# Kernel tuning notes

Measured on AMD Instinct MI355X. Metric: run time of the kernel, lower is better.

The kernel has to match this reference:

```python
import jax, jax.numpy as jnp
import numpy as np

NUM_NODES = 100000
NUM_EDGES = 1600000
NUM_GRAPHS = 64
NUM_FEATURES = 128
DIM = 128
OUTPUT_SIZE = 16


def setup_inputs() -> dict:
    key = jax.random.key(0)
    ks = jax.random.split(key, 7)
    features = jax.random.normal(ks[0], (NUM_NODES, NUM_FEATURES), dtype=jnp.float32)
    W1 = jax.random.normal(ks[1], (NUM_FEATURES, DIM), dtype=jnp.float32) / np.sqrt(NUM_FEATURES)
    W2 = jax.random.normal(ks[2], (DIM, DIM), dtype=jnp.float32) / np.sqrt(DIM)
    W3 = jax.random.normal(ks[3], (DIM, OUTPUT_SIZE), dtype=jnp.float32) / np.sqrt(DIM)
    src = jax.random.randint(ks[4], (NUM_EDGES,), 0, NUM_NODES, dtype=jnp.int32)
    dst = jax.random.randint(ks[5], (NUM_EDGES,), 0, NUM_NODES, dtype=jnp.int32)
    graph_ids = jnp.sort(jax.random.randint(ks[6], (NUM_NODES,), 0, NUM_GRAPHS, dtype=jnp.int32))
    return {"features": features, "W1": W1, "W2": W2, "W3": W3,
            "src": src, "dst": dst, "graph_ids": graph_ids}


def _graph_conv(x, W, src, dst, num_nodes):
    # DGL GraphConv, norm='none', bias=False: h_v = sum_{u -> v} (x_u @ W)
    xw = x @ W                      # [N, dim]
    msg = xw[src]                   # gather per edge [E, dim]
    return jax.ops.segment_sum(msg, dst, num_segments=num_nodes)


def reference(features, W1, W2, W3, src, dst, graph_ids):
    n = features.shape[0]
    h = jax.nn.relu(_graph_conv(features, W1, src, dst, n))  # conv1 + ReLU
    h = _graph_conv(h, W2, src, dst, n)                      # conv2
    # dgl.mean_nodes: per-graph mean over nodes
    sums = jax.ops.segment_sum(h, graph_ids, num_segments=NUM_GRAPHS)          # [G, dim]
    counts = jax.ops.segment_sum(jnp.ones((n,), h.dtype), graph_ids,
                                 num_segments=NUM_GRAPHS)                       # [G]
    pooled = sums / jnp.maximum(counts, 1.0)[:, None]
    out = pooled @ W3                                         # fc1 (no bias)
    return jax.nn.sigmoid(out)                                # torch.sigmoid activation
```

## Files before the change

### kernel.cpp

```cpp
#include <hip/hip_runtime.h>

#define NXCD 8
#define PA_NB 256
#define CSLOT 32
#define OVCAP 65536

typedef short bf16x8 __attribute__((ext_vector_type(8)));
typedef float f32x4  __attribute__((ext_vector_type(4)));
typedef unsigned int u32x2 __attribute__((ext_vector_type(2)));
typedef unsigned int u32x4 __attribute__((ext_vector_type(4)));

union U4S8 { uint4 u; u32x4 v; bf16x8 s; };

__device__ __forceinline__ unsigned int f2bf(float f) {
    unsigned int u = __float_as_uint(f);
    return (u + 0x7fffu + ((u >> 16) & 1u)) >> 16;
}
__device__ __forceinline__ float bflo(unsigned int u) { return __uint_as_float(u << 16); }
__device__ __forceinline__ float bfhi(unsigned int u) { return __uint_as_float(u & 0xffff0000u); }

__device__ __forceinline__ f32x4 nt_ld_f4(const float4* p) {
    return __builtin_nontemporal_load((const f32x4*)p);
}
__device__ __forceinline__ u32x2 nt_ld_u2(const uint2* p) {
    return __builtin_nontemporal_load((const u32x2*)p);
}
__device__ __forceinline__ unsigned int nt_ld_u(const unsigned int* p) {
    return __builtin_nontemporal_load(p);
}

__global__ __launch_bounds__(256) void fconv(
    const float4* __restrict__ F4, uint4* __restrict__ B4, long long n8)
{
    long long t = (long long)blockIdx.x * 256 + threadIdx.x;
    if (t >= n8) return;
    f32x4 a = nt_ld_f4(&F4[2 * t]);
    f32x4 b = nt_ld_f4(&F4[2 * t + 1]);
    uint4 o;
    o.x = f2bf(a.x) | (f2bf(a.y) << 16);
    o.y = f2bf(a.z) | (f2bf(a.w) << 16);
    o.z = f2bf(b.x) | (f2bf(b.y) << 16);
    o.w = f2bf(b.z) | (f2bf(b.w) << 16);
    B4[t] = o;
}

__global__ __launch_bounds__(256) void fillfix_xcd(
    const int* __restrict__ src, const int* __restrict__ dst,
    int* __restrict__ cnt, int* __restrict__ col,
    int* __restrict__ ovd, int* __restrict__ ovs, int* __restrict__ ov_cnt,
    int E, int N)
{
    int x  = blockIdx.x & (NXCD - 1);
    int bi = blockIdx.x >> 3;
    int K  = gridDim.x >> 3;
    int chunk = (N + NXCD - 1) / NXCD;
    int lo = x * chunk;
    int hi = lo + chunk; if (hi > N) hi = N;
    for (int e = bi * 256 + threadIdx.x; e < E; e += K * 256) {
        int d = dst[e];
        int s = src[e];
        if (d >= lo && d < hi) {
            int pos = atomicAdd(&cnt[d], 1);
            if (pos < CSLOT) {
                col[(size_t)d * CSLOT + pos] = s;
            } else {
                int op = atomicAdd(ov_cnt, 1);
                if (op < OVCAP) { ovd[op] = d; ovs[op] = s; }
            }
        }
    }
}

__global__ __launch_bounds__(256) void edge_pa(
    const int* __restrict__ src, const int* __restrict__ dst,
    const int* __restrict__ gid, unsigned int* __restrict__ PA32, int E, int N)
{
    int x  = blockIdx.x & (NXCD - 1);
    int bi = blockIdx.x >> 3;
    int K  = gridDim.x >> 3;
    int chunk = (N + NXCD - 1) / NXCD;
    int lo = x * chunk;
    int hi = lo + chunk; if (hi > N) hi = N;
    for (int e = bi * 256 + threadIdx.x; e < E; e += K * 256) {
        int s = src[e];
        int d = dst[e];
        if (s >= lo && s < hi) {
            int g = gid[d];
            atomicAdd(&PA32[(size_t)s * 16 + (g >> 2)], 1u << ((g & 3) * 8));
        }
    }
}

__global__ __launch_bounds__(256) void csr_agg_bf16(
    const uint4* __restrict__ X, const int* __restrict__ cnt,
    const int* __restrict__ col,
    const int* __restrict__ ovd, const int* __restrict__ ovs,
    const int* __restrict__ ov_cnt,
    uint4* __restrict__ T, int N)
{
    int v = blockIdx.x * 16 + (threadIdx.x >> 4);
    if (v >= N) return;
    int lane = threadIdx.x & 15;
    int c = cnt[v];
    int end = c < CSLOT ? c : CSLOT;
    const int* cb = col + (size_t)v * CSLOT;
    float a0=0,a1=0,a2=0,a3=0,a4=0,a5=0,a6=0,a7=0;
    #define ACCUM(u) { \
        a0 += bflo((u).x); a1 += bfhi((u).x); \
        a2 += bflo((u).y); a3 += bfhi((u).y); \
        a4 += bflo((u).z); a5 += bfhi((u).z); \
        a6 += bflo((u).w); a7 += bfhi((u).w); }
    int i = 0;
    for (; i + 1 < end; i += 2) {
        int c0 = cb[i], c1 = cb[i + 1];
        uint4 x0 = X[(size_t)c0 * 16 + lane];
        uint4 x1 = X[(size_t)c1 * 16 + lane];
        ACCUM(x0) ACCUM(x1)
    }
    if (i < end) {
        uint4 x0 = X[(size_t)cb[i] * 16 + lane];
        ACCUM(x0)
    }
    int oc = *ov_cnt; if (oc > OVCAP) oc = OVCAP;
    for (int k = 0; k < oc; ++k) {
        if (ovd[k] == v) {
            uint4 x0 = X[(size_t)ovs[k] * 16 + lane];
            ACCUM(x0)
        }
    }
    #undef ACCUM
    uint4 o;
    o.x = f2bf(a0) | (f2bf(a1) << 16);
    o.y = f2bf(a2) | (f2bf(a3) << 16);
    o.z = f2bf(a4) | (f2bf(a5) << 16);
    o.w = f2bf(a6) | (f2bf(a7) << 16);
    T[(size_t)v * 16 + lane] = o;
}

__global__ __launch_bounds__(256) void gemm_mfma(
    const uint4* __restrict__ T, const float* __restrict__ W,
    uint2* __restrict__ Y, int N, int RB)
{
    __shared__ char sWT[32768];
    int t = threadIdx.x;
    {
        int c = t & 127;
        int xo = (c & 7) << 4;
        #pragma unroll
        for (int i = 0; i < 8; ++i) {
            int kc = (t >> 7) + 2 * i;
            int k0 = kc * 8;
            unsigned int h[8];
            #pragma unroll
            for (int j = 0; j < 8; ++j)
                h[j] = f2bf(W[(k0 + j) * 128 + c]);
            uint4 pk;
            pk.x = h[0] | (h[1] << 16);
            pk.y = h[2] | (h[3] << 16);
            pk.z = h[4] | (h[5] << 16);
            pk.w = h[6] | (h[7] << 16);
            *(uint4*)(sWT + c * 256 + ((k0 * 2) ^ xo)) = pk;
        }
    }
    __syncthreads();

    int wid = t >> 6, l = t & 63;
    int rb = blockIdx.x * 4 + wid;
    if (rb >= RB) return;
    int lrow = l & 15, lg = l >> 4;
    int row = rb * 16 + lrow;

    U4S8 cv;
    bf16x8 a[4];
    #pragma unroll
    for (int kk = 0; kk < 4; ++kk) {
        cv.u = (row < N) ? T[(size_t)row * 16 + kk * 4 + lg] : make_uint4(0,0,0,0);
        a[kk] = cv.s;
    }

    f32x4 acc[8];
    #pragma unroll
    for (int ct = 0; ct < 8; ++ct) acc[ct] = (f32x4){0.f,0.f,0.f,0.f};

    #pragma unroll
    for (int ct = 0; ct < 8; ++ct) {
        int c = ct * 16 + lrow;
        const char* base = sWT + c * 256;
        int xo = (c & 7) << 4;
        #pragma unroll
        for (int kk = 0; kk < 4; ++kk) {
            cv.u = *(const uint4*)(base + ((kk * 64 + lg * 16) ^ xo));
            acc[ct] = __builtin_amdgcn_mfma_f32_16x16x32_bf16(a[kk], cv.s, acc[ct], 0, 0, 0);
        }
    }

    #pragma unroll
    for (int ct = 0; ct < 8; ++ct) {
        uint2 o;
        o.x = f2bf(fmaxf(acc[ct][0], 0.f)) | (f2bf(fmaxf(acc[ct][1], 0.f)) << 16);
        o.y = f2bf(fmaxf(acc[ct][2], 0.f)) | (f2bf(fmaxf(acc[ct][3], 0.f)) << 16);
        Y[((size_t)rb * 8 + ct) * 64 + l] = o;
    }
}

__global__ __launch_bounds__(256) void pa_gemm(
    const uint2* __restrict__ Ybf, const unsigned int* __restrict__ PA32,
    float4* __restrict__ partial, int N, int chunk)
{
    __shared__ float sY[8 * 128];
    __shared__ unsigned int sPA[8 * 16];

    int b = blockIdx.x;
    int v0 = b * chunk;
    int v1 = v0 + chunk; if (v1 > N) v1 = N;

    int t = threadIdx.x;
    int j = t & 15, dgrp = t >> 4;
    float4 acc[4][2];
    #pragma unroll
    for (int i = 0; i < 4; ++i) { acc[i][0] = make_float4(0,0,0,0); acc[i][1] = make_float4(0,0,0,0); }

    int ctS = t >> 5, lsub = t & 31;
    int vlocS = (lsub >> 4) * 4;
    int cS = ctS * 16 + (lsub & 15);

    for (int vc = v0; vc < v1; vc += 8) {
        {
            int rb = vc >> 4, qb = vc & 15;
            u32x2 u = nt_ld_u2(&Ybf[((size_t)rb * 8 + ctS) * 64 + (qb >> 2) * 16 + lsub]);
            sY[(vlocS + 0) * 128 + cS] = bflo(u.x);
            sY[(vlocS + 1) * 128 + cS] = bfhi(u.x);
            sY[(vlocS + 2) * 128 + cS] = bflo(u.y);
            sY[(vlocS + 3) * 128 + cS] = bfhi(u.y);
        }
        if (t < 128) {
            int vp = vc + (t >> 4);
            sPA[t] = (vp < v1) ? nt_ld_u(&PA32[(size_t)vp * 16 + (t & 15)]) : 0u;
        }
        __syncthreads();
        const float4* sY4 = (const float4*)sY;
        #pragma unroll
        for (int vv = 0; vv < 8; ++vv) {
            unsigned int pw = sPA[vv * 16 + j];
            float4 y0 = sY4[vv * 32 + dgrp * 2 + 0];
            float4 y1 = sY4[vv * 32 + dgrp * 2 + 1];
            #pragma unroll
            for (int i = 0; i < 4; ++i) {
                float w = (float)((pw >> (i * 8)) & 0xffu);
                acc[i][0].x += w * y0.x; acc[i][0].y += w * y0.y;
                acc[i][0].z += w * y0.z; acc[i][0].w += w * y0.w;
                acc[i][1].x += w * y1.x; acc[i][1].y += w * y1.y;
                acc[i][1].z += w * y1.z; acc[i][1].w += w * y1.w;
            }
        }
        __syncthreads();
    }

    #pragma unroll
    for (int i = 0; i < 4; ++i) {
        int g = j * 4 + i;
        partial[(size_t)b * 2048 + g * 32 + dgrp * 2 + 0] = acc[i][0];
        partial[(size_t)b * 2048 + g * 32 + dgrp * 2 + 1] = acc[i][1];
    }
}

__global__ __launch_bounds__(256) void reduce_partial(
    const float* __restrict__ partial, float* __restrict__ pooled)
{
    int o = blockIdx.x * 256 + threadIdx.x;
    float s = 0.f;
    #pragma unroll 4
    for (int b = 0; b < PA_NB; ++b)
        s += partial[(size_t)b * 8192 + o];
    pooled[o] = s;
}

__global__ __launch_bounds__(1024) void final_fused(
    const float* __restrict__ pooled, const int* __restrict__ gid, int N,
    const float* __restrict__ W2, const float* __restrict__ W3,
    float* __restrict__ out)
{
    __shared__ float sW23[128 * 16];
    __shared__ int lb[65];
    int t = threadIdx.x;
    if (t <= 64) {
        int lo = 0, hi = N;
        while (lo < hi) { int mid = (lo + hi) >> 1; if (gid[mid] < t) lo = mid + 1; else hi = mid; }
        lb[t] = lo;
    }
    for (int idx = t; idx < 2048; idx += 1024) {
        int k = idx >> 4, o = idx & 15;
        float a = 0.f;
        #pragma unroll 16
        for (int jj = 0; jj < 128; ++jj)
            a += W2[k * 128 + jj] * W3[jj * 16 + o];
        sW23[idx] = a;
    }
    __syncthreads();
    int g = t >> 4, o = t & 15;
    float cnt = fmaxf((float)(lb[g + 1] - lb[g]), 1.0f);
    float acc = 0.f;
    #pragma unroll 16
    for (int k = 0; k < 128; ++k)
        acc += pooled[g * 128 + k] * sW23[k * 16 + o];
    acc /= cnt;
    out[g * 16 + o] = 1.0f / (1.0f + __expf(-acc));
}

extern "C" void kernel_launch(void* const* d_in, const int* in_sizes, int n_in,
                              void* d_out, int out_size, void* d_ws, size_t ws_size,
                              hipStream_t stream)
{
    const float* features = (const float*)d_in[0];
    const float* W1       = (const float*)d_in[1];
    const float* W2       = (const float*)d_in[2];
    const float* W3       = (const float*)d_in[3];
    const int*   src      = (const int*)d_in[4];
    const int*   dst      = (const int*)d_in[5];
    const int*   gid      = (const int*)d_in[6];
    int N = in_sizes[0] / 128;
    int E = in_sizes[4];
    float* out = (float*)d_out;

    int RB = (N + 15) / 16;

    char* ws = (char*)d_ws;
    size_t p = 0;
    auto alloc = [&](size_t bytes) { void* r = ws + p; p = (p + bytes + 255) & ~(size_t)255; return r; };
    unsigned int* fbf  = (unsigned int*)alloc((size_t)N * 128 * 2);
    unsigned int* tbf  = (unsigned int*)alloc((size_t)N * 128 * 2);
    uint2*        Ybf  = (uint2*)alloc((size_t)RB * 8 * 64 * 8);
    unsigned int* PA32 = (unsigned int*)alloc((size_t)N * 16 * 4);
    float* partial = (float*)alloc((size_t)PA_NB * 8192 * 4);
    float* pooled  = (float*)alloc(64 * 128 * sizeof(float));
    int*   cnt     = (int*)alloc((size_t)N * sizeof(int));
    int*   col     = (int*)alloc((size_t)N * CSLOT * sizeof(int));
    int*   ovd     = (int*)alloc((size_t)OVCAP * sizeof(int));
    int*   ovs     = (int*)alloc((size_t)OVCAP * sizeof(int));
    int*   ov_cnt  = (int*)alloc(256);

    int aggGrid  = (N + 15) / 16;
    int xcdGrid  = 2048;
    int gGrid    = (RB + 3) / 4;
    int paChunk  = (((N + PA_NB - 1) / PA_NB) + 15) & ~15;
    long long n8 = (long long)N * 16;

    fconv<<<(int)((n8 + 255) / 256), 256, 0, stream>>>((const float4*)features, (uint4*)fbf, n8);

    (void)hipMemsetAsync(cnt, 0, (size_t)N * sizeof(int), stream);
    (void)hipMemsetAsync(ov_cnt, 0, 256, stream);
    (void)hipMemsetAsync(PA32, 0, (size_t)N * 16 * 4, stream);
    fillfix_xcd<<<xcdGrid, 256, 0, stream>>>(src, dst, cnt, col, ovd, ovs, ov_cnt, E, N);
    edge_pa<<<xcdGrid, 256, 0, stream>>>(src, dst, gid, PA32, E, N);

    csr_agg_bf16<<<aggGrid, 256, 0, stream>>>((const uint4*)fbf, cnt, col, ovd, ovs, ov_cnt, (uint4*)tbf, N);
    gemm_mfma<<<gGrid, 256, 0, stream>>>((const uint4*)tbf, W1, Ybf, N, RB);

    pa_gemm<<<PA_NB, 256, 0, stream>>>(Ybf, PA32, (float4*)partial, N, paChunk);
    reduce_partial<<<32, 256, 0, stream>>>(partial, pooled);

    final_fused<<<1, 1024, 0, stream>>>(pooled, gid, N, W2, W3, out);
}
```

Measured before the change: 341.3 us.

## Replace per-node graph-count matrix with direct edge-wise pooled gather into shared atomics

After: 1.285 ms. +276.7%, slower.

```diff
diff --git a/kernel.cpp b/kernel.cpp
--- a/kernel.cpp
+++ b/kernel.cpp
@@ -1,7 +1,7 @@
 #include <hip/hip_runtime.h>
 
 #define NXCD 8
-#define PA_NB 256
+#define EP_NB 1024
 #define CSLOT 32
 #define OVCAP 65536
 
@@ -21,12 +21,6 @@
 
 __device__ __forceinline__ f32x4 nt_ld_f4(const float4* p) {
     return __builtin_nontemporal_load((const f32x4*)p);
-}
-__device__ __forceinline__ u32x2 nt_ld_u2(const uint2* p) {
-    return __builtin_nontemporal_load((const u32x2*)p);
-}
-__device__ __forceinline__ unsigned int nt_ld_u(const unsigned int* p) {
-    return __builtin_nontemporal_load(p);
 }
 
 __global__ __launch_bounds__(256) void fconv(
@@ -58,8 +52,8 @@
     int hi = lo + chunk; if (hi > N) hi = N;
     for (int e = bi * 256 + threadIdx.x; e < E; e += K * 256) {
         int d = dst[e];
-        int s = src[e];
         if (d >= lo && d < hi) {
+            int s = src[e];
             int pos = atomicAdd(&cnt[d], 1);
             if (pos < CSLOT) {
                 col[(size_t)d * CSLOT + pos] = s;
@@ -67,26 +61,6 @@
                 int op = atomicAdd(ov_cnt, 1);
                 if (op < OVCAP) { ovd[op] = d; ovs[op] = s; }
             }
-        }
-    }
-}
-
-__global__ __launch_bounds__(256) void edge_pa(
-    const int* __restrict__ src, const int* __restrict__ dst,
-    const int* __restrict__ gid, unsigned int* __restrict__ PA32, int E, int N)
-{
-    int x  = blockIdx.x & (NXCD - 1);
-    int bi = blockIdx.x >> 3;
-    int K  = gridDim.x >> 3;
-    int chunk = (N + NXCD - 1) / NXCD;
-    int lo = x * chunk;
-    int hi = lo + chunk; if (hi > N) hi = N;
-    for (int e = bi * 256 + threadIdx.x; e < E; e += K * 256) {
-        int s = src[e];
-        int d = dst[e];
-        if (s >= lo && s < hi) {
-            int g = gid[d];
-            atomicAdd(&PA32[(size_t)s * 16 + (g >> 2)], 1u << ((g & 3) * 8));
         }
     }
 }
@@ -139,9 +113,10 @@
 
 __global__ __launch_bounds__(256) void gemm_mfma(
     const uint4* __restrict__ T, const float* __restrict__ W,
-    uint2* __restrict__ Y, int N, int RB)
+    uint4* __restrict__ Y2q, int N, int RB)
 {
     __shared__ char sWT[32768];
+    __shared__ unsigned short sT[4][16 * 128];
     int t = threadIdx.x;
     {
         int c = t & 127;
@@ -194,74 +169,67 @@
         }
     }
 
+    unsigned short* st = sT[wid];
     #pragma unroll
     for (int ct = 0; ct < 8; ++ct) {
-        uint2 o;
-        o.x = f2bf(fmaxf(acc[ct][0], 0.f)) | (f2bf(fmaxf(acc[ct][1], 0.f)) << 16);
-        o.y = f2bf(fmaxf(acc[ct][2], 0.f)) | (f2bf(fmaxf(acc[ct][3], 0.f)) << 16);
-        Y[((size_t)rb * 8 + ct) * 64 + l] = o;
-    }
-}
-
-__global__ __launch_bounds__(256) void pa_gemm(
-    const uint2* __restrict__ Ybf, const unsigned int* __restrict__ PA32,
-    float4* __restrict__ partial, int N, int chunk)
-{
-    __shared__ float sY[8 * 128];
-    __shared__ unsigned int sPA[8 * 16];
-
-    int b = blockIdx.x;
-    int v0 = b * chunk;
-    int v1 = v0 + chunk; if (v1 > N) v1 = N;
-
+        #pragma unroll
+        for (int r4 = 0; r4 < 4; ++r4)
+            st[(lg * 4 + r4) * 128 + ct * 16 + lrow] =
+                (unsigned short)f2bf(fmaxf(acc[ct][r4], 0.f));
+    }
+    #pragma unroll
+    for (int r = 0; r < 4; ++r) {
+        int rr = r * 4 + lg;
+        uint4 q = *(const uint4*)(st + rr * 128 + lrow * 8);
+        Y2q[((size_t)rb * 16 + rr) * 16 + lrow] = q;
+    }
+}
+
+__global__ __launch_bounds__(256) void edge_pool(
+    const int* __restrict__ src, const int* __restrict__ dst,
+    const int* __restrict__ gid, const unsigned int* __restrict__ Y2u,
+    float4* __restrict__ partial, int E)
+{
+    __shared__ float sp[64 * 128];
     int t = threadIdx.x;
-    int j = t & 15, dgrp = t >> 4;
-    float4 acc[4][2];
-    #pragma unroll
-    for (int i = 0; i < 4; ++i) { acc[i][0] = make_float4(0,0,0,0); acc[i][1] = make_float4(0,0,0,0); }
-
-    int ctS = t >> 5, lsub = t & 31;
-    int vlocS = (lsub >> 4) * 4;
-    int cS = ctS * 16 + (lsub & 15);
-
-    for (int vc = v0; vc < v1; vc += 8) {
-        {
-            int rb = vc >> 4, qb = vc & 15;
-            u32x2 u = nt_ld_u2(&Ybf[((size_t)rb * 8 + ctS) * 64 + (qb >> 2) * 16 + lsub]);
-            sY[(vlocS + 0) * 128 + cS] = bflo(u.x);
-            sY[(vlocS + 1) * 128 + cS] = bfhi(u.x);
-            sY[(vlocS + 2) * 128 + cS] = bflo(u.y);
-            sY[(vlocS + 3) * 128 + cS] = bfhi(u.y);
-        }
-        if (t < 128) {
-            int vp = vc + (t >> 4);
-            sPA[t] = (vp < v1) ? nt_ld_u(&PA32[(size_t)vp * 16 + (t & 15)]) : 0u;
-        }
-        __syncthreads();
-        const float4* sY4 = (const float4*)sY;
-        #pragma unroll
-        for (int vv = 0; vv < 8; ++vv) {
-            unsigned int pw = sPA[vv * 16 + j];
-            float4 y0 = sY4[vv * 32 + dgrp * 2 + 0];
-            float4 y1 = sY4[vv * 32 + dgrp * 2 + 1];
-            #pragma unroll
-            for (int i = 0; i < 4; ++i) {
-                float w = (float)((pw >> (i * 8)) & 0xffu);
-                acc[i][0].x += w * y0.x; acc[i][0].y += w * y0.y;
-                acc[i][0].z += w * y0.z; acc[i][0].w += w * y0.w;
-                acc[i][1].x += w * y1.x; acc[i][1].y += w * y1.y;
-                acc[i][1].z += w * y1.z; acc[i][1].w += w * y1.w;
-            }
-        }
-        __syncthreads();
-    }
-
-    #pragma unroll
-    for (int i = 0; i < 4; ++i) {
-        int g = j * 4 + i;
-        partial[(size_t)b * 2048 + g * 32 + dgrp * 2 + 0] = acc[i][0];
-        partial[(size_t)b * 2048 + g * 32 + dgrp * 2 + 1] = acc[i][1];
-    }
+    #pragma unroll
+    for (int i = t; i < 8192; i += 256) sp[i] = 0.f;
+    __syncthreads();
+
+    int l = t & 63;
+    int w = (blockIdx.x << 2) | (t >> 6);
+    const int STRIDE = EP_NB * 4 * 4;
+
+    for (int e0 = w * 4; e0 < E; e0 += STRIDE) {
+        int d0 = -1, d1 = -1, d2 = -1, d3 = -1;
+        int s0 = 0, s1 = 0, s2 = 0, s3 = 0;
+        if (e0 + 0 < E) { d0 = dst[e0 + 0]; s0 = src[e0 + 0]; }
+        if (e0 + 1 < E) { d1 = dst[e0 + 1]; s1 = src[e0 + 1]; }
+        if (e0 + 2 < E) { d2 = dst[e0 + 2]; s2 = src[e0 + 2]; }
+        if (e0 + 3 < E) { d3 = dst[e0 + 3]; s3 = src[e0 + 3]; }
+        int g0 = (d0 >= 0) ? gid[d0] : 0;
+        int g1 = (d1 >= 0) ? gid[d1] : 0;
+        int g2 = (d2 >= 0) ? gid[d2] : 0;
+        int g3 = (d3 >= 0) ? gid[d3] : 0;
+        unsigned y0 = (d0 >= 0) ? Y2u[(size_t)s0 * 64 + l] : 0u;
+        unsigned y1 = (d1 >= 0) ? Y2u[(size_t)s1 * 64 + l] : 0u;
+        unsigned y2 = (d2 >= 0) ? Y2u[(size_t)s2 * 64 + l] : 0u;
+        unsigned y3 = (d3 >= 0) ? Y2u[(size_t)s3 * 64 + l] : 0u;
+        if (d0 >= 0) { atomicAdd(&sp[g0 * 128 + 2 * l], bflo(y0));
+                       atomicAdd(&sp[g0 * 128 + 2 * l + 1], bfhi(y0)); }
+        if (d1 >= 0) { atomicAdd(&sp[g1 * 128 + 2 * l], bflo(y1));
+                       atomicAdd(&sp[g1 * 128 + 2 * l + 1], bfhi(y1)); }
+        if (d2 >= 0) { atomicAdd(&sp[g2 * 128 + 2 * l], bflo(y2));
+                       atomicAdd(&sp[g2 * 128 + 2 * l + 1], bfhi(y2)); }
+        if (d3 >= 0) { atomicAdd(&sp[g3 * 128 + 2 * l], bflo(y3));
+                       atomicAdd(&sp[g3 * 128 + 2 * l + 1], bfhi(y3)); }
+    }
+    __syncthreads();
+
+    const float4* sp4 = (const float4*)sp;
+    #pragma unroll
+    for (int i = t; i < 2048; i += 256)
+        partial[(size_t)blockIdx.x * 2048 + i] = sp4[i];
 }
 
 __global__ __launch_bounds__(256) void reduce_partial(
@@ -270,7 +238,7 @@
     int o = blockIdx.x * 256 + threadIdx.x;
     float s = 0.f;
     #pragma unroll 4
-    for (int b = 0; b < PA_NB; ++b)
+    for (int b = 0; b < EP_NB; ++b)
         s += partial[(size_t)b * 8192 + o];
     pooled[o] = s;
 }
@@ -329,34 +297,30 @@
     auto alloc = [&](size_t bytes) { void* r = ws + p; p = (p + bytes + 255) & ~(size_t)255; return r; };
     unsigned int* fbf  = (unsigned int*)alloc((size_t)N * 128 * 2);
     unsigned int* tbf  = (unsigned int*)alloc((size_t)N * 128 * 2);
-    uint2*        Ybf  = (uint2*)alloc((size_t)RB * 8 * 64 * 8);
-    unsigned int* PA32 = (unsigned int*)alloc((size_t)N * 16 * 4);
-    float* partial = (float*)alloc((size_t)PA_NB * 8192 * 4);
+    uint4*        Y2q  = (uint4*)alloc((size_t)RB * 16 * 128 * 2);
     float* pooled  = (float*)alloc(64 * 128 * sizeof(float));
     int*   cnt     = (int*)alloc((size_t)N * sizeof(int));
     int*   col     = (int*)alloc((size_t)N * CSLOT * sizeof(int));
     int*   ovd     = (int*)alloc((size_t)OVCAP * sizeof(int));
     int*   ovs     = (int*)alloc((size_t)OVCAP * sizeof(int));
     int*   ov_cnt  = (int*)alloc(256);
+    float* partial = (float*)fbf;
 
     int aggGrid  = (N + 15) / 16;
     int xcdGrid  = 2048;
     int gGrid    = (RB + 3) / 4;
-    int paChunk  = (((N + PA_NB - 1) / PA_NB) + 15) & ~15;
     long long n8 = (long long)N * 16;
 
     fconv<<<(int)((n8 + 255) / 256), 256, 0, stream>>>((const float4*)features, (uint4*)fbf, n8);
 
     (void)hipMemsetAsync(cnt, 0, (size_t)N * sizeof(int), stream);
     (void)hipMemsetAsync(ov_cnt, 0, 256, stream);
-    (void)hipMemsetAsync(PA32, 0, (size_t)N * 16 * 4, stream);
     fillfix_xcd<<<xcdGrid, 256, 0, stream>>>(src, dst, cnt, col, ovd, ovs, ov_cnt, E, N);
-    edge_pa<<<xcdGrid, 256, 0, stream>>>(src, dst, gid, PA32, E, N);
 
     csr_agg_bf16<<<aggGrid, 256, 0, stream>>>((const uint4*)fbf, cnt, col, ovd, ovs, ov_cnt, (uint4*)tbf, N);
-    gemm_mfma<<<gGrid, 256, 0, stream>>>((const uint4*)tbf, W1, Ybf, N, RB);
-
-    pa_gemm<<<PA_NB, 256, 0, stream>>>(Ybf, PA32, (float4*)partial, N, paChunk);
+    gemm_mfma<<<gGrid, 256, 0, stream>>>((const uint4*)tbf, W1, Y2q, N, RB);
+
+    edge_pool<<<EP_NB, 256, 0, stream>>>(src, dst, gid, (const unsigned int*)Y2q, (float4*)partial, E);
     reduce_partial<<<32, 256, 0, stream>>>(partial, pooled);
 
     final_fused<<<1, 1024, 0, stream>>>(pooled, gid, N, W2, W3, out);
```

## Fuse CSR fill and PA histogram edge passes into one kernel, merge memsets

Applied to the files above, without the earlier changes.

After: 329.8 us. -3.4%, faster.

```diff
diff --git a/kernel.cpp b/kernel.cpp
--- a/kernel.cpp
+++ b/kernel.cpp
@@ -44,11 +44,12 @@
     B4[t] = o;
 }
 
-__global__ __launch_bounds__(256) void fillfix_xcd(
+__global__ __launch_bounds__(256) void edge_build_xcd(
     const int* __restrict__ src, const int* __restrict__ dst,
+    const int* __restrict__ gid,
     int* __restrict__ cnt, int* __restrict__ col,
     int* __restrict__ ovd, int* __restrict__ ovs, int* __restrict__ ov_cnt,
-    int E, int N)
+    unsigned int* __restrict__ PA32, int E, int N)
 {
     int x  = blockIdx.x & (NXCD - 1);
     int bi = blockIdx.x >> 3;
@@ -59,6 +60,10 @@
     for (int e = bi * 256 + threadIdx.x; e < E; e += K * 256) {
         int d = dst[e];
         int s = src[e];
+        if (s >= lo && s < hi) {
+            int g = gid[d];
+            atomicAdd(&PA32[(size_t)s * 16 + (g >> 2)], 1u << ((g & 3) * 8));
+        }
         if (d >= lo && d < hi) {
             int pos = atomicAdd(&cnt[d], 1);
             if (pos < CSLOT) {
@@ -67,26 +72,6 @@
                 int op = atomicAdd(ov_cnt, 1);
                 if (op < OVCAP) { ovd[op] = d; ovs[op] = s; }
             }
-        }
-    }
-}
-
-__global__ __launch_bounds__(256) void edge_pa(
-    const int* __restrict__ src, const int* __restrict__ dst,
-    const int* __restrict__ gid, unsigned int* __restrict__ PA32, int E, int N)
-{
-    int x  = blockIdx.x & (NXCD - 1);
-    int bi = blockIdx.x >> 3;
-    int K  = gridDim.x >> 3;
-    int chunk = (N + NXCD - 1) / NXCD;
-    int lo = x * chunk;
-    int hi = lo + chunk; if (hi > N) hi = N;
-    for (int e = bi * 256 + threadIdx.x; e < E; e += K * 256) {
-        int s = src[e];
-        int d = dst[e];
-        if (s >= lo && s < hi) {
-            int g = gid[d];
-            atomicAdd(&PA32[(size_t)s * 16 + (g >> 2)], 1u << ((g & 3) * 8));
         }
     }
 }
@@ -330,14 +315,17 @@
     unsigned int* fbf  = (unsigned int*)alloc((size_t)N * 128 * 2);
     unsigned int* tbf  = (unsigned int*)alloc((size_t)N * 128 * 2);
     uint2*        Ybf  = (uint2*)alloc((size_t)RB * 8 * 64 * 8);
-    unsigned int* PA32 = (unsigned int*)alloc((size_t)N * 16 * 4);
     float* partial = (float*)alloc((size_t)PA_NB * 8192 * 4);
     float* pooled  = (float*)alloc(64 * 128 * sizeof(float));
-    int*   cnt     = (int*)alloc((size_t)N * sizeof(int));
-    int*   col     = (int*)alloc((size_t)N * CSLOT * sizeof(int));
-    int*   ovd     = (int*)alloc((size_t)OVCAP * sizeof(int));
-    int*   ovs     = (int*)alloc((size_t)OVCAP * sizeof(int));
-    int*   ov_cnt  = (int*)alloc(256);
+    size_t paB  = (size_t)N * 16 * 4;
+    size_t cntB = (((size_t)N * 4) + 255) & ~(size_t)255;
+    char*  zr   = (char*)alloc(paB + cntB + 256);
+    unsigned int* PA32 = (unsigned int*)zr;
+    int*   cnt    = (int*)(zr + paB);
+    int*   ov_cnt = (int*)(zr + paB + cntB);
+    int*   col    = (int*)alloc((size_t)N * CSLOT * sizeof(int));
+    int*   ovd    = (int*)alloc((size_t)OVCAP * sizeof(int));
+    int*   ovs    = (int*)alloc((size_t)OVCAP * sizeof(int));
 
     int aggGrid  = (N + 15) / 16;
     int xcdGrid  = 2048;
@@ -347,11 +335,8 @@
 
     fconv<<<(int)((n8 + 255) / 256), 256, 0, stream>>>((const float4*)features, (uint4*)fbf, n8);
 
-    (void)hipMemsetAsync(cnt, 0, (size_t)N * sizeof(int), stream);
-    (void)hipMemsetAsync(ov_cnt, 0, 256, stream);
-    (void)hipMemsetAsync(PA32, 0, (size_t)N * 16 * 4, stream);
-    fillfix_xcd<<<xcdGrid, 256, 0, stream>>>(src, dst, cnt, col, ovd, ovs, ov_cnt, E, N);
-    edge_pa<<<xcdGrid, 256, 0, stream>>>(src, dst, gid, PA32, E, N);
+    (void)hipMemsetAsync(zr, 0, paB + cntB + 256, stream);
+    edge_build_xcd<<<xcdGrid, 256, 0, stream>>>(src, dst, gid, cnt, col, ovd, ovs, ov_cnt, PA32, E, N);
 
     csr_agg_bf16<<<aggGrid, 256, 0, stream>>>((const uint4*)fbf, cnt, col, ovd, ovs, ov_cnt, (uint4*)tbf, N);
     gemm_mfma<<<gGrid, 256, 0, stream>>>((const uint4*)tbf, W1, Ybf, N, RB);
```
